# Kernel optimization log

Measured on AMD Instinct MI355X. Metric: run time of the kernel, lower is better.

## Reference

```python
import jax, jax.numpy as jnp
import numpy as np

N = 20000      # nodes
E = 640000     # directed edges
NB = 124       # n_atom_basis
FD = NB + 4    # feature dim after res_embed concat = 128
RBF = 16
CUTOFF = 10.0
NCONV = 3
SCF = FD + 10  # sidechain torsion feature dim = 138

act = jax.nn.silu  # 'swish'

def _w(key, shape, fan_in):
    return jax.random.normal(key, shape, jnp.float32) / np.sqrt(fan_in)

def setup_inputs() -> dict:
    key = jax.random.key(0)
    ks = iter(jax.random.split(key, 64))
    cg_z = jax.random.randint(next(ks), (N,), 0, 25)
    cg_xyz = jax.random.normal(next(ks), (N, 3), jnp.float32) * 4.0
    src = jax.random.randint(next(ks), (E,), 0, N)
    off = jax.random.randint(next(ks), (E,), 1, N)
    dst = (src + off) % N  # no self-loops -> dist > 0
    CG_nbr_list = jnp.stack([src, dst], axis=1)
    mapping = jax.random.randint(next(ks), (N,), 0, N)  # unused by forward
    S = jax.random.normal(next(ks), (N, NB), jnp.float32)
    p = {}
    p['res_embed'] = _w(next(ks), (25, 4), 1.0)
    p['msg_W1'] = _w(next(ks), (NCONV, FD, FD), FD); p['msg_b1'] = jnp.zeros((NCONV, FD))
    p['msg_W2'] = _w(next(ks), (NCONV, FD, FD), FD); p['msg_b2'] = jnp.zeros((NCONV, FD))
    p['dist_W'] = _w(next(ks), (NCONV, RBF, FD), RBF); p['dist_b'] = jnp.zeros((NCONV, FD))
    p['dense_W1'] = _w(next(ks), (NCONV, FD, FD), FD); p['dense_b1'] = jnp.zeros((NCONV, FD))
    p['dense_W2'] = _w(next(ks), (NCONV, FD, FD), FD); p['dense_b2'] = jnp.zeros((NCONV, FD))
    p['bb_dist_emb'] = _w(next(ks), (25, 3), 1.0)
    p['sc_dist_emb'] = _w(next(ks), (25, 10), 1.0)
    p['bba_W1'] = _w(next(ks), (FD, 3), FD); p['bba_b1'] = jnp.zeros((3,))
    p['bba_W2'] = _w(next(ks), (3, 3), 3);  p['bba_b2'] = jnp.zeros((3,))
    p['sca_W1'] = _w(next(ks), (FD, 10), FD); p['sca_b1'] = jnp.zeros((10,))
    p['sca_W2'] = _w(next(ks), (10, 10), 10); p['sca_b2'] = jnp.zeros((10,))
    p['bbt_W1'] = _w(next(ks), (FD + 3, 3), FD + 3); p['bbt_b1'] = jnp.zeros((3,))
    p['bbt_W2'] = _w(next(ks), (3, 3), 3); p['bbt_b2'] = jnp.zeros((3,))
    p['sct_W1'] = _w(next(ks), (NCONV, SCF, SCF), SCF); p['sct_b1'] = jnp.zeros((NCONV, SCF))
    p['sct_W2'] = _w(next(ks), (NCONV, SCF, SCF), SCF); p['sct_b2'] = jnp.zeros((NCONV, SCF))
    p['ft_W1'] = _w(next(ks), (SCF, 10), SCF); p['ft_b1'] = jnp.zeros((10,))
    p['ft_W2'] = _w(next(ks), (10, 10), 10); p['ft_b2'] = jnp.zeros((10,))
    return dict(cg_z=cg_z, cg_xyz=cg_xyz, CG_nbr_list=CG_nbr_list, mapping=mapping, S=S, **p)

def reference(cg_z, cg_xyz, CG_nbr_list, mapping, S, res_embed,
              msg_W1, msg_b1, msg_W2, msg_b2, dist_W, dist_b,
              dense_W1, dense_b1, dense_W2, dense_b2,
              bb_dist_emb, sc_dist_emb,
              bba_W1, bba_b1, bba_W2, bba_b2,
              sca_W1, sca_b1, sca_W2, sca_b2,
              bbt_W1, bbt_b1, bbt_W2, bbt_b2,
              sct_W1, sct_b1, sct_W2, sct_b2,
              ft_W1, ft_b1, ft_W2, ft_b2):
    nbr = CG_nbr_list  # already directed (both i>j and j>i present)
    i_idx, j_idx = nbr[:, 0], nbr[:, 1]
    r_ij = cg_xyz[j_idx] - cg_xyz[i_idx]             # [E,3]
    dist = jnp.linalg.norm(r_ij, axis=-1)            # [E]
    # PaiNN radial basis: sin(n*pi*d/cutoff)/d, n=1..RBF
    n_arr = jnp.arange(1, RBF + 1, dtype=jnp.float32)
    rbf = jnp.sin(dist[:, None] * n_arr * (jnp.pi / CUTOFF)) / dist[:, None]  # [E,RBF]
    env = jnp.where(dist < CUTOFF, 0.5 * (jnp.cos(jnp.pi * dist / CUTOFF) + 1.0), 0.0)[:, None]
    S = jnp.concatenate([S, res_embed[cg_z]], axis=-1)  # [N,FD]
    for i in range(NCONV):
        phi = act(S @ msg_W1[i] + msg_b1[i]) @ msg_W2[i] + msg_b2[i]   # [N,FD]
        w_s = (rbf @ dist_W[i] + dist_b[i]) * env                      # [E,FD]
        msg = phi[j_idx] * w_s                                         # gather + per-edge message
        v = jax.ops.segment_sum(msg, i_idx, num_segments=N)            # scatter-add
        h = act(act(v) @ dense_W1[i] + dense_b1[i]) @ dense_W2[i] + dense_b2[i]
        S = S + h
    bb_angle = act(act(S) @ bba_W1 + bba_b1) @ bba_W2 + bba_b2          # [N,3]
    bbt_in = jnp.concatenate([S, bb_angle], axis=-1)
    bb_torsion = act(act(bbt_in) @ bbt_W1 + bbt_b1) @ bbt_W2 + bbt_b2   # [N,3]
    sc_angle = act(act(S) @ sca_W1 + sca_b1) @ sca_W2 + sca_b2          # [N,10]
    sc_S = jnp.concatenate([S, sc_angle], axis=-1)                      # [N,SCF]
    for i in range(NCONV):
        sc_S = sc_S + (act(act(sc_S) @ sct_W1[i] + sct_b1[i]) @ sct_W2[i] + sct_b2[i])
    sc_torsion = act(act(sc_S) @ ft_W1 + ft_b1) @ ft_W2 + ft_b2         # [N,10]
    bb_dist = bb_dist_emb[cg_z][..., None]                              # [N,3,1]
    sc_dist = sc_dist_emb[cg_z][..., None]                              # [N,10,1]
    ic_bb = jnp.concatenate([bb_dist, bb_angle[..., None], bb_torsion[..., None]], axis=-1)  # [N,3,3]
    ic_sc = jnp.concatenate([sc_dist, sc_angle[..., None], sc_torsion[..., None]], axis=-1)  # [N,10,3]
    ic_recon = jnp.concatenate([ic_bb, ic_sc], axis=-2)                 # [N,13,3]
    return ic_recon
```

## Files before the change

kernel.cpp:

```cpp
#include <hip/hip_runtime.h>
#include <hip/hip_bf16.h>

#define DIV_UP(a,b) (((a)+(b)-1)/(b))

typedef __attribute__((ext_vector_type(8))) short bf16x8;
typedef __attribute__((ext_vector_type(4))) float f32x4;

__device__ __forceinline__ float silu_f(float x) {
    return x / (1.0f + __expf(-x));
}
__device__ __forceinline__ unsigned short f2bf(float x) {
    __hip_bfloat16 h = __float2bfloat16(x);
    return *reinterpret_cast<unsigned short*>(&h);
}
__device__ __forceinline__ float bf2f(unsigned short u) {
    unsigned int v = (unsigned int)u << 16;
    return __uint_as_float(v);
}
__device__ __forceinline__ void split_bf(float x, unsigned short& hi, unsigned short& lo) {
    hi = f2bf(x);
    lo = f2bf(x - bf2f(hi));
}
__device__ __forceinline__ bf16x8 pack8(unsigned int w0, unsigned int w1,
                                        unsigned int w2, unsigned int w3) {
    union { unsigned int u[4]; bf16x8 v; } t;
    t.u[0] = w0; t.u[1] = w1; t.u[2] = w2; t.u[3] = w3;
    return t.v;
}

#define WSLOT 16384

__global__ __launch_bounds__(256) void prep_weights_kernel(
    const float* __restrict__ msgW1, const float* __restrict__ msgW2,
    const float* __restrict__ denseW1, const float* __restrict__ denseW2,
    unsigned short* __restrict__ WB)
{
    int slot = blockIdx.y;
    int kind = slot / 3, conv = slot % 3;
    const float* base;
    switch (kind) {
        case 0: base = msgW1; break;
        case 1: base = msgW2; break;
        case 2: base = denseW1; break;
        default: base = denseW2; break;
    }
    const float* W = base + (size_t)conv * 128 * 128;
    int idx = blockIdx.x * 256 + threadIdx.x;
    if (idx >= 16384) return;
    int c = idx >> 7, k = idx & 127;
    float val = W[(size_t)k * 128 + c];
    unsigned short hi, lo;
    split_bf(val, hi, lo);
    WB[(size_t)(2 * slot) * WSLOT + idx]     = hi;
    WB[(size_t)(2 * slot + 1) * WSLOT + idx] = lo;
}

__global__ __launch_bounds__(256) void hist_kernel(
    const int* __restrict__ nbr, int* __restrict__ counts, int E)
{
    int e = blockIdx.x * 256 + threadIdx.x;
    if (e < E) atomicAdd(&counts[nbr[2 * e]], 1);
}

__global__ __launch_bounds__(1024) void scan_kernel(
    const int* __restrict__ counts, int* __restrict__ peptr, int N)
{
    __shared__ int part[1024];
    const int t = threadIdx.x;
    const int chunk = DIV_UP(N, 1024);
    int s = 0;
    for (int c = 0; c < chunk; ++c) {
        int idx = t * chunk + c;
        if (idx < N) s += (counts[idx] + 31) & ~31;
    }
    part[t] = s;
    __syncthreads();
    for (int off = 1; off < 1024; off <<= 1) {
        int v = (t >= off) ? part[t - off] : 0;
        __syncthreads();
        part[t] += v;
        __syncthreads();
    }
    int pre = (t > 0) ? part[t - 1] : 0;
    for (int c = 0; c < chunk; ++c) {
        int idx = t * chunk + c;
        if (idx < N) { peptr[idx] = pre; pre += (counts[idx] + 31) & ~31; }
    }
    if (t == 1023) peptr[N] = part[1023];
}

__global__ __launch_bounds__(256) void geom_scatter_kernel(
    const int* __restrict__ nbr, const float* __restrict__ xyz,
    const int* __restrict__ peptr, int* __restrict__ cursor,
    unsigned short* __restrict__ rbfT, unsigned short* __restrict__ envs,
    int* __restrict__ js, int E)
{
    int e = blockIdx.x * 256 + threadIdx.x;
    if (e >= E) return;
    int i = nbr[2 * e], j = nbr[2 * e + 1];
    float dx = xyz[3 * j + 0] - xyz[3 * i + 0];
    float dy = xyz[3 * j + 1] - xyz[3 * i + 1];
    float dz = xyz[3 * j + 2] - xyz[3 * i + 2];
    float dist = sqrtf(dx * dx + dy * dy + dz * dz);
    float x = dist * 0.3141592653589793f;
    float s, c;
    __sincosf(x, &s, &c);
    float env = (dist < 10.0f) ? 0.5f * (c + 1.0f) : 0.0f;
    float inv_env = env / dist;
    float two_c = 2.0f * c;
    float sm1 = 0.0f, s0 = s;
    __align__(16) unsigned short ob[16];
    #pragma unroll
    for (int k = 0; k < 16; ++k) {
        ob[k] = f2bf(s0 * inv_env);
        float s1 = two_c * s0 - sm1;
        sm1 = s0; s0 = s1;
    }
    int p = peptr[i] + atomicAdd(&cursor[i], 1);
    uint4* rp = (uint4*)(rbfT + (size_t)p * 16);
    rp[0] = *(const uint4*)&ob[0];
    rp[1] = *(const uint4*)&ob[8];
    envs[p] = f2bf(env);
    js[p] = j;
}

__global__ __launch_bounds__(256) void repack_kernel(
    unsigned short* __restrict__ rbfT, int nchunks)
{
    __shared__ __align__(16) unsigned short T[4][512];
    const int wave = threadIdx.x >> 6;
    const int lane = threadIdx.x & 63;
    const int c = blockIdx.x * 4 + wave;
    const bool act = (c < nchunks);
    if (act)
        *(uint4*)&T[wave][lane * 8] = *(const uint4*)(rbfT + (size_t)c * 512 + lane * 8);
    __syncthreads();
    if (act) {
        const int lg = lane >> 4, l15 = lane & 15;
        __align__(16) unsigned short o[8];
        #pragma unroll
        for (int i = 0; i < 8; ++i)
            o[i] = T[wave][(8 * lg + i) * 16 + l15];
        *(uint4*)(rbfT + (size_t)c * 512 + lane * 8) = *(const uint4*)o;
    }
}

__global__ __launch_bounds__(256) void concat_s_kernel(
    const float* __restrict__ S, const float* __restrict__ res_embed,
    const int* __restrict__ z, float* __restrict__ S0, int N)
{
    int idx = blockIdx.x * 256 + threadIdx.x;
    if (idx >= N * 128) return;
    int n = idx >> 7, c = idx & 127;
    float val = (c < 124) ? S[n * 124 + c] : res_embed[z[n] * 4 + (c - 124)];
    S0[idx] = val;
}

template<int MT, bool PREACT, bool RESID, typename OutT>
__global__ __launch_bounds__(256) void mlp2_mfma_kernel(
    const float* __restrict__ X,
    const unsigned short* __restrict__ W1hi, const unsigned short* __restrict__ W1lo,
    const float* __restrict__ b1,
    const unsigned short* __restrict__ W2hi, const unsigned short* __restrict__ W2lo,
    const float* __restrict__ b2,
    OutT* __restrict__ Y, int nrows)
{
    constexpr int RB   = MT / 16;
    constexpr int ROWB = 256;
    __shared__ __align__(16) unsigned short XHhi[MT * 128];
    __shared__ __align__(16) unsigned short XHlo[MT * 128];
    __shared__ __align__(16) unsigned short WS[128 * 128];

    const int tid  = threadIdx.x;
    const int wave = tid >> 6;
    const int lane = tid & 63;
    const int l15  = lane & 15;
    const int kg   = lane >> 4;
    const int row0 = blockIdx.x * MT;

    for (int idx = tid; idx < MT * 32; idx += 256) {
        int r = idx >> 5, q = idx & 31;
        int gr = row0 + r;
        float4 xv = make_float4(0.f, 0.f, 0.f, 0.f);
        if (gr < nrows) xv = *(const float4*)(X + (size_t)gr * 128 + 4 * q);
        if (PREACT) { xv.x = silu_f(xv.x); xv.y = silu_f(xv.y);
                      xv.z = silu_f(xv.z); xv.w = silu_f(xv.w); }
        ushort4 h, l;
        split_bf(xv.x, h.x, l.x); split_bf(xv.y, h.y, l.y);
        split_bf(xv.z, h.z, l.z); split_bf(xv.w, h.w, l.w);
        int off = (8 * q) ^ ((r & 7) << 4);
        *(ushort4*)((char*)XHhi + r * ROWB + off) = h;
        *(ushort4*)((char*)XHlo + r * ROWB + off) = l;
    }

    f32x4 acc[RB][2];

    #define STAGE_W(WPTR)                                                       \
        for (int idx = tid; idx < 2048; idx += 256) {                           \
            int r = idx >> 4;                                                   \
            int byt = (idx & 15) * 16;                                          \
            *(uint4*)((char*)WS + r * ROWB + (byt ^ ((r & 7) << 4))) =          \
                *(const uint4*)((WPTR) + (size_t)idx * 8);                      \
        }

    #define PASS(WITH_LO)                                                       \
        _Pragma("unroll")                                                       \
        for (int kk = 0; kk < 4; ++kk) {                                        \
            const int kbyte = kk * 64 + kg * 16;                                \
            bf16x8 ah[RB], al[RB];                                              \
            _Pragma("unroll")                                                   \
            for (int rb = 0; rb < RB; ++rb) {                                   \
                int r = 16 * rb + l15;                                          \
                int off = kbyte ^ ((r & 7) << 4);                               \
                ah[rb] = *(const bf16x8*)((const char*)XHhi + r * ROWB + off);  \
                if (WITH_LO)                                                    \
                    al[rb] = *(const bf16x8*)((const char*)XHlo + r * ROWB + off); \
            }                                                                   \
            _Pragma("unroll")                                                   \
            for (int cbi = 0; cbi < 2; ++cbi) {                                 \
                int rw = 16 * (wave + 4 * cbi) + l15;                           \
                int offw = kbyte ^ ((rw & 7) << 4);                             \
                bf16x8 bw = *(const bf16x8*)((const char*)WS + rw * ROWB + offw); \
                _Pragma("unroll")                                               \
                for (int rb = 0; rb < RB; ++rb) {                               \
                    f32x4 t = acc[rb][cbi];                                     \
                    t = __builtin_amdgcn_mfma_f32_16x16x32_bf16(ah[rb], bw, t, 0, 0, 0); \
                    if (WITH_LO)                                                \
                        t = __builtin_amdgcn_mfma_f32_16x16x32_bf16(al[rb], bw, t, 0, 0, 0); \
                    acc[rb][cbi] = t;                                           \
                }                                                               \
            }                                                                   \
        }

    #pragma unroll
    for (int a = 0; a < RB; ++a) { acc[a][0] = (f32x4){0,0,0,0}; acc[a][1] = (f32x4){0,0,0,0}; }
    STAGE_W(W1hi)
    __syncthreads();
    PASS(true)
    __syncthreads();
    STAGE_W(W1lo)
    __syncthreads();
    PASS(false)
    __syncthreads();

    #pragma unroll
    for (int cbi = 0; cbi < 2; ++cbi) {
        int col = 16 * (wave + 4 * cbi) + l15;
        float b1v = b1[col];
        #pragma unroll
        for (int rb = 0; rb < RB; ++rb)
            #pragma unroll
            for (int i = 0; i < 4; ++i) {
                int r = 16 * rb + kg * 4 + i;
                float h = silu_f(acc[rb][cbi][i] + b1v);
                unsigned short hh, hl;
                split_bf(h, hh, hl);
                int off = (2 * col) ^ ((r & 7) << 4);
                *(unsigned short*)((char*)XHhi + r * ROWB + off) = hh;
                *(unsigned short*)((char*)XHlo + r * ROWB + off) = hl;
            }
    }
    #pragma unroll
    for (int a = 0; a < RB; ++a) { acc[a][0] = (f32x4){0,0,0,0}; acc[a][1] = (f32x4){0,0,0,0}; }
    STAGE_W(W2hi)
    __syncthreads();
    PASS(true)
    __syncthreads();
    STAGE_W(W2lo)
    __syncthreads();
    PASS(false)
    #undef PASS
    #undef STAGE_W

    #pragma unroll
    for (int cbi = 0; cbi < 2; ++cbi) {
        int col = 16 * (wave + 4 * cbi) + l15;
        float b2v = b2[col];
        #pragma unroll
        for (int rb = 0; rb < RB; ++rb)
            #pragma unroll
            for (int i = 0; i < 4; ++i) {
                int gr = row0 + 16 * rb + kg * 4 + i;
                if (gr < nrows) {
                    size_t off = (size_t)gr * 128 + col;
                    float val = acc[rb][cbi][i] + b2v;
                    if (RESID) val += (float)Y[off];
                    if constexpr (sizeof(OutT) == 2)
                        Y[off] = __float2bfloat16(val);
                    else
                        Y[off] = val;
                }
            }
    }
}

template<int K, int ROWS, int RR, bool PREACT, bool RESID, typename OutT>
__global__ __launch_bounds__(256) void mlp2_kernel(
    const float* __restrict__ X, int ldX,
    const float* __restrict__ W1, const float* __restrict__ b1,
    const float* __restrict__ W2, const float* __restrict__ b2,
    OutT* __restrict__ Y, int ldY, int nrows)
{
    constexpr int NC = (K + 31) / 32;
    __shared__ float Xs[ROWS * K];
    __shared__ float Hs[ROWS * K];
    const int tid = threadIdx.x;
    const int row0 = blockIdx.x * ROWS;

    for (int idx = tid; idx < ROWS * K; idx += 256) {
        int r = idx / K, c = idx - r * K;
        int gr = row0 + r;
        float x = (gr < nrows) ? X[(size_t)gr * ldX + c] : 0.0f;
        if (PREACT) x = silu_f(x);
        Xs[idx] = x;
    }
    __syncthreads();

    const int cc = tid & 31;
    const int r0 = (tid >> 5) * RR;

    float acc[NC][RR];
    #pragma unroll
    for (int jc = 0; jc < NC; ++jc) {
        int col = cc + 32 * jc;
        float bv = (col < K) ? b1[col] : 0.0f;
        #pragma unroll
        for (int rr = 0; rr < RR; ++rr) acc[jc][rr] = bv;
    }
    for (int k = 0; k < K; ++k) {
        float w[NC];
        #pragma unroll
        for (int jc = 0; jc < NC; ++jc) {
            int col = cc + 32 * jc;
            w[jc] = (col < K) ? W1[k * K + col] : 0.0f;
        }
        float xv[RR];
        #pragma unroll
        for (int rr = 0; rr < RR; ++rr) xv[rr] = Xs[(r0 + rr) * K + k];
        #pragma unroll
        for (int jc = 0; jc < NC; ++jc)
            #pragma unroll
            for (int rr = 0; rr < RR; ++rr)
                acc[jc][rr] = fmaf(xv[rr], w[jc], acc[jc][rr]);
    }
    #pragma unroll
    for (int jc = 0; jc < NC; ++jc) {
        int col = cc + 32 * jc;
        if (col < K) {
            #pragma unroll
            for (int rr = 0; rr < RR; ++rr)
                Hs[(r0 + rr) * K + col] = silu_f(acc[jc][rr]);
        }
    }
    __syncthreads();

    #pragma unroll
    for (int jc = 0; jc < NC; ++jc) {
        int col = cc + 32 * jc;
        float bv = (col < K) ? b2[col] : 0.0f;
        #pragma unroll
        for (int rr = 0; rr < RR; ++rr) acc[jc][rr] = bv;
    }
    for (int k = 0; k < K; ++k) {
        float w[NC];
        #pragma unroll
        for (int jc = 0; jc < NC; ++jc) {
            int col = cc + 32 * jc;
            w[jc] = (col < K) ? W2[k * K + col] : 0.0f;
        }
        float xv[RR];
        #pragma unroll
        for (int rr = 0; rr < RR; ++rr) xv[rr] = Hs[(r0 + rr) * K + k];
        #pragma unroll
        for (int jc = 0; jc < NC; ++jc)
            #pragma unroll
            for (int rr = 0; rr < RR; ++rr)
                acc[jc][rr] = fmaf(xv[rr], w[jc], acc[jc][rr]);
    }
    #pragma unroll
    for (int jc = 0; jc < NC; ++jc) {
        int col = cc + 32 * jc;
        if (col < K) {
            #pragma unroll
            for (int rr = 0; rr < RR; ++rr) {
                int gr = row0 + r0 + rr;
                if (gr < nrows) {
                    size_t off = (size_t)gr * ldY + col;
                    float val = acc[jc][rr];
                    if (RESID) val += (float)Y[off];
                    if constexpr (sizeof(OutT) == 2)
                        Y[off] = __float2bfloat16(val);
                    else
                        Y[off] = val;
                }
            }
        }
    }
}

__global__ __launch_bounds__(256) void gather_mfma_kernel(
    const int* __restrict__ peptr,
    const unsigned short* __restrict__ rbfT,
    const unsigned short* __restrict__ envs,
    const int* __restrict__ js,
    const unsigned short* __restrict__ phi,
    const float* __restrict__ distW, const float* __restrict__ distb,
    float* __restrict__ v, int N)
{
    const int wv = blockIdx.x * 4 + (threadIdx.x >> 6);
    const int lane = threadIdx.x & 63;
    const int n = wv >> 1;
    const int h = wv & 1;
    if (n >= N) return;
    const int l15 = lane & 15;
    const int lg  = lane >> 4;

    f32x4 acc[4];
    float eac[4];
    #pragma unroll
    for (int cb = 0; cb < 4; ++cb) { acc[cb] = (f32x4){0,0,0,0}; eac[cb] = 0.f; }

    const int p0 = peptr[n], p1 = peptr[n + 1];

    for (int p = p0; p < p1; p += 32) {
        bf16x8 af = *(const bf16x8*)(rbfT + (size_t)(p >> 5) * 512 + lane * 8);

        bf16x8 a2f = (bf16x8){0,0,0,0,0,0,0,0};
        if (l15 == 0)
            a2f = *(const bf16x8*)(envs + p + 8 * lg);

        int4 j03 = *(const int4*)(js + p + 8 * lg);
        int4 j47 = *(const int4*)(js + p + 8 * lg + 4);

        const unsigned short* pb0 = phi + (size_t)j03.x * 128 + 64 * h + l15;
        const unsigned short* pb1 = phi + (size_t)j03.y * 128 + 64 * h + l15;
        const unsigned short* pb2 = phi + (size_t)j03.z * 128 + 64 * h + l15;
        const unsigned short* pb3 = phi + (size_t)j03.w * 128 + 64 * h + l15;
        const unsigned short* pb4 = phi + (size_t)j47.x * 128 + 64 * h + l15;
        const unsigned short* pb5 = phi + (size_t)j47.y * 128 + 64 * h + l15;
        const unsigned short* pb6 = phi + (size_t)j47.z * 128 + 64 * h + l15;
        const unsigned short* pb7 = phi + (size_t)j47.w * 128 + 64 * h + l15;

        #pragma unroll
        for (int cbi = 0; cbi < 4; ++cbi) {
            const int o = cbi * 16;
            unsigned int b0 = (unsigned int)pb0[o] | ((unsigned int)pb1[o] << 16);
            unsigned int b1 = (unsigned int)pb2[o] | ((unsigned int)pb3[o] << 16);
            unsigned int b2 = (unsigned int)pb4[o] | ((unsigned int)pb5[o] << 16);
            unsigned int b3 = (unsigned int)pb6[o] | ((unsigned int)pb7[o] << 16);
            bf16x8 bf = pack8(b0, b1, b2, b3);
            acc[cbi] = __builtin_amdgcn_mfma_f32_16x16x32_bf16(af, bf, acc[cbi], 0, 0, 0);
            f32x4 z = (f32x4){0, 0, 0, 0};
            z = __builtin_amdgcn_mfma_f32_16x16x32_bf16(a2f, bf, z, 0, 0, 0);
            eac[cbi] += z[0];
        }
    }

    #pragma unroll
    for (int cbi = 0; cbi < 4; ++cbi) {
        int col = 64 * h + cbi * 16 + l15;
        float part = acc[cbi][0] * distW[(lg * 4 + 0) * 128 + col];
        part = fmaf(acc[cbi][1], distW[(lg * 4 + 1) * 128 + col], part);
        part = fmaf(acc[cbi][2], distW[(lg * 4 + 2) * 128 + col], part);
        part = fmaf(acc[cbi][3], distW[(lg * 4 + 3) * 128 + col], part);
        if (lg == 0) part = fmaf(eac[cbi], distb[col], part);
        part += __shfl_xor(part, 16, 64);
        part += __shfl_xor(part, 32, 64);
        if (lane < 16) v[(size_t)n * 128 + col] = part;
    }
}

__global__ __launch_bounds__(256) void fused_heads_kernel(
    const float* __restrict__ S0,
    const float* __restrict__ bbaW1, const float* __restrict__ bbab1,
    const float* __restrict__ bbaW2, const float* __restrict__ bbab2,
    const float* __restrict__ bbtW1, const float* __restrict__ bbtb1,
    const float* __restrict__ bbtW2, const float* __restrict__ bbtb2,
    const float* __restrict__ scaW1, const float* __restrict__ scab1,
    const float* __restrict__ scaW2, const float* __restrict__ scab2,
    float* __restrict__ bbA, float* __restrict__ bbT,
    float* __restrict__ scA, float* __restrict__ scS, int N)
{
    const int wid = threadIdx.x >> 6;
    const int lane = threadIdx.x & 63;
    const int n = blockIdx.x * 4 + wid;
    if (n >= N) return;

    float x0 = S0[(size_t)n * 128 + lane];
    float x1 = S0[(size_t)n * 128 + 64 + lane];
    float s0 = silu_f(x0), s1 = silu_f(x1);

    float ba[3];
    #pragma unroll
    for (int m = 0; m < 3; ++m)
        ba[m] = fmaf(s0, bbaW1[lane * 3 + m], s1 * bbaW1[(lane + 64) * 3 + m]);
    #pragma unroll
    for (int m = 0; m < 3; ++m)
        #pragma unroll
        for (int off = 32; off > 0; off >>= 1)
            ba[m] += __shfl_xor(ba[m], off, 64);
    float bbo[3];
    {
        float tm[3];
        #pragma unroll
        for (int m = 0; m < 3; ++m) tm[m] = silu_f(ba[m] + bbab1[m]);
        #pragma unroll
        for (int mm = 0; mm < 3; ++mm) {
            float o = bbab2[mm];
            #pragma unroll
            for (int m = 0; m < 3; ++m) o = fmaf(tm[m], bbaW2[m * 3 + mm], o);
            bbo[mm] = o;
        }
    }
    if (lane < 3) {
        float ov = bbo[0];
        if (lane == 1) ov = bbo[1];
        if (lane == 2) ov = bbo[2];
        bbA[(size_t)n * 3 + lane] = ov;
    }

    float bt[3];
    #pragma unroll
    for (int m = 0; m < 3; ++m)
        bt[m] = fmaf(s0, bbtW1[lane * 3 + m], s1 * bbtW1[(lane + 64) * 3 + m]);
    #pragma unroll
    for (int m = 0; m < 3; ++m)
        #pragma unroll
        for (int off = 32; off > 0; off >>= 1)
            bt[m] += __shfl_xor(bt[m], off, 64);
    #pragma unroll
    for (int m = 0; m < 3; ++m)
        #pragma unroll
        for (int t = 0; t < 3; ++t)
            bt[m] = fmaf(silu_f(bbo[t]), bbtW1[(128 + t) * 3 + m], bt[m]);
    {
        float tm[3], bto[3];
        #pragma unroll
        for (int m = 0; m < 3; ++m) tm[m] = silu_f(bt[m] + bbtb1[m]);
        #pragma unroll
        for (int mm = 0; mm < 3; ++mm) {
            float o = bbtb2[mm];
            #pragma unroll
            for (int m = 0; m < 3; ++m) o = fmaf(tm[m], bbtW2[m * 3 + mm], o);
            bto[mm] = o;
        }
        if (lane < 3) {
            float ov = bto[0];
            if (lane == 1) ov = bto[1];
            if (lane == 2) ov = bto[2];
            bbT[(size_t)n * 3 + lane] = ov;
        }
    }

    float sa[10];
    #pragma unroll
    for (int m = 0; m < 10; ++m)
        sa[m] = fmaf(s0, scaW1[lane * 10 + m], s1 * scaW1[(lane + 64) * 10 + m]);
    #pragma unroll
    for (int m = 0; m < 10; ++m)
        #pragma unroll
        for (int off = 32; off > 0; off >>= 1)
            sa[m] += __shfl_xor(sa[m], off, 64);
    float sco[10];
    {
        float tm[10];
        #pragma unroll
        for (int m = 0; m < 10; ++m) tm[m] = silu_f(sa[m] + scab1[m]);
        #pragma unroll
        for (int mm = 0; mm < 10; ++mm) {
            float o = scab2[mm];
            #pragma unroll
            for (int m = 0; m < 10; ++m) o = fmaf(tm[m], scaW2[m * 10 + mm], o);
            sco[mm] = o;
        }
    }
    float scv = sco[0];
    #pragma unroll
    for (int m = 1; m < 10; ++m)
        if (lane == m) scv = sco[m];
    if (lane < 10) scA[(size_t)n * 10 + lane] = scv;

    scS[(size_t)n * 140 + lane] = x0;
    scS[(size_t)n * 140 + 64 + lane] = x1;
    if (lane < 12) scS[(size_t)n * 140 + 128 + lane] = (lane < 10) ? scv : 0.0f;
}

template<int M>
__global__ __launch_bounds__(256) void head_kernel(
    const float* __restrict__ X, int ldX, int K1,
    const float* __restrict__ X2, int ldX2, int K2,
    const float* __restrict__ W1, const float* __restrict__ b1,
    const float* __restrict__ W2, const float* __restrict__ b2,
    float* __restrict__ out, int ldOut, int nrows)
{
    const int wid = threadIdx.x >> 6;
    const int lane = threadIdx.x & 63;
    const int n = blockIdx.x * 4 + wid;
    if (n >= nrows) return;
    const int K = K1 + K2;
    float sx[3];
    #pragma unroll
    for (int t = 0; t < 3; ++t) {
        int k = lane + 64 * t;
        float v = 0.0f;
        if (k < K1) v = X[(size_t)n * ldX + k];
        else if (k < K) v = X2[(size_t)n * ldX2 + (k - K1)];
        sx[t] = (k < K) ? silu_f(v) : 0.0f;
    }
    float acc[M];
    #pragma unroll
    for (int m = 0; m < M; ++m) {
        float a = 0.0f;
        #pragma unroll
        for (int t = 0; t < 3; ++t) {
            int k = lane + 64 * t;
            if (k < K) a = fmaf(sx[t], W1[k * M + m], a);
        }
        acc[m] = a;
    }
    #pragma unroll
    for (int m = 0; m < M; ++m) {
        #pragma unroll
        for (int off = 32; off > 0; off >>= 1)
            acc[m] += __shfl_xor(acc[m], off, 64);
    }
    float tm[M];
    #pragma unroll
    for (int m = 0; m < M; ++m) tm[m] = silu_f(acc[m] + b1[m]);
    if (lane < M) {
        float o = b2[lane];
        #pragma unroll
        for (int m = 0; m < M; ++m) o = fmaf(tm[m], W2[m * M + lane], o);
        out[(size_t)n * ldOut + lane] = o;
    }
}

__global__ __launch_bounds__(256) void assemble_kernel(
    const int* __restrict__ z,
    const float* __restrict__ bbde, const float* __restrict__ scde,
    const float* __restrict__ bbA, const float* __restrict__ bbT,
    const float* __restrict__ scA, const float* __restrict__ scT,
    float* __restrict__ out, int N)
{
    int idx = blockIdx.x * 256 + threadIdx.x;
    if (idx >= N * 39) return;
    int n = idx / 39;
    int s = idx - n * 39;
    int row = s / 3;
    int col = s - row * 3;
    float val;
    if (row < 3) {
        if (col == 0)      val = bbde[z[n] * 3 + row];
        else if (col == 1) val = bbA[n * 3 + row];
        else               val = bbT[n * 3 + row];
    } else {
        int r = row - 3;
        if (col == 0)      val = scde[z[n] * 10 + r];
        else if (col == 1) val = scA[n * 10 + r];
        else               val = scT[n * 10 + r];
    }
    out[idx] = val;
}

extern "C" void kernel_launch(void* const* d_in, const int* in_sizes, int n_in,
                              void* d_out, int out_size, void* d_ws, size_t ws_size,
                              hipStream_t stream)
{
    const int*   cg_z        = (const int*)d_in[0];
    const float* cg_xyz      = (const float*)d_in[1];
    const int*   nbr         = (const int*)d_in[2];
    const float* S_in        = (const float*)d_in[4];
    const float* res_embed   = (const float*)d_in[5];
    const float* msg_W1      = (const float*)d_in[6];
    const float* msg_b1      = (const float*)d_in[7];
    const float* msg_W2      = (const float*)d_in[8];
    const float* msg_b2      = (const float*)d_in[9];
    const float* dist_W      = (const float*)d_in[10];
    const float* dist_b      = (const float*)d_in[11];
    const float* dense_W1    = (const float*)d_in[12];
    const float* dense_b1    = (const float*)d_in[13];
    const float* dense_W2    = (const float*)d_in[14];
    const float* dense_b2    = (const float*)d_in[15];
    const float* bb_dist_emb = (const float*)d_in[16];
    const float* sc_dist_emb = (const float*)d_in[17];
    const float* bba_W1      = (const float*)d_in[18];
    const float* bba_b1      = (const float*)d_in[19];
    const float* bba_W2      = (const float*)d_in[20];
    const float* bba_b2      = (const float*)d_in[21];
    const float* sca_W1      = (const float*)d_in[22];
    const float* sca_b1      = (const float*)d_in[23];
    const float* sca_W2      = (const float*)d_in[24];
    const float* sca_b2      = (const float*)d_in[25];
    const float* bbt_W1      = (const float*)d_in[26];
    const float* bbt_b1      = (const float*)d_in[27];
    const float* bbt_W2      = (const float*)d_in[28];
    const float* bbt_b2      = (const float*)d_in[29];
    const float* sct_W1      = (const float*)d_in[30];
    const float* sct_b1      = (const float*)d_in[31];
    const float* sct_W2      = (const float*)d_in[32];
    const float* sct_b2      = (const float*)d_in[33];
    const float* ft_W1       = (const float*)d_in[34];
    const float* ft_b1       = (const float*)d_in[35];
    const float* ft_W2       = (const float*)d_in[36];
    const float* ft_b2       = (const float*)d_in[37];

    const int N = in_sizes[0];
    const int E = in_sizes[2] / 2;
    const int EPAD = ((E + 31 * N) / 32) * 32 + 32;

    unsigned short* WB   = (unsigned short*)d_ws;
    unsigned short* rbfT = WB + (size_t)24 * WSLOT;
    unsigned short* envs = rbfT + (size_t)EPAD * 16;
    int*            js   = (int*)(envs + (size_t)EPAD);
    float* ws   = (float*)(js + (size_t)EPAD);
    float* S0   = ws;  ws += (size_t)N * 128;
    float* V    = ws;  ws += (size_t)N * 128;
    float* scS  = ws;  ws += (size_t)N * 140;
    float* bbA  = ws;  ws += (size_t)N * 3;
    float* bbT  = ws;  ws += (size_t)N * 3;
    float* scA  = ws;  ws += (size_t)N * 10;
    float* scT  = ws;  ws += (size_t)N * 10;
    __hip_bfloat16* PHI = (__hip_bfloat16*)ws;  ws += (size_t)N * 64;
    int* peptr  = (int*)ws;  ws = (float*)((int*)ws + (N + 1));
    int* counts = (int*)ws;  ws = (float*)((int*)ws + N);
    int* cursor = (int*)ws;  ws = (float*)((int*)ws + N);

    (void)hipMemsetAsync(rbfT, 0, (size_t)EPAD * 38, stream);
    (void)hipMemsetAsync(counts, 0, (size_t)2 * N * sizeof(int), stream);

    prep_weights_kernel<<<dim3(64, 12), 256, 0, stream>>>(
        msg_W1, msg_W2, dense_W1, dense_W2, WB);

    hist_kernel<<<DIV_UP(E, 256), 256, 0, stream>>>(nbr, counts, E);
    scan_kernel<<<1, 1024, 0, stream>>>(counts, peptr, N);
    geom_scatter_kernel<<<DIV_UP(E, 256), 256, 0, stream>>>(
        nbr, cg_xyz, peptr, cursor, rbfT, envs, js, E);
    const int nchunks = EPAD / 32;
    repack_kernel<<<DIV_UP(nchunks, 4), 256, 0, stream>>>(rbfT, nchunks);

    concat_s_kernel<<<DIV_UP(N * 128, 256), 256, 0, stream>>>(S_in, res_embed, cg_z, S0, N);

    #define WHI(kind, conv) (WB + (size_t)(2 * ((kind) * 3 + (conv))) * WSLOT)
    #define WLO(kind, conv) (WB + (size_t)(2 * ((kind) * 3 + (conv)) + 1) * WSLOT)

    for (int i = 0; i < 3; ++i) {
        mlp2_mfma_kernel<48, false, false, __hip_bfloat16>
            <<<DIV_UP(N, 48), 256, 0, stream>>>(
            S0, WHI(0, i), WLO(0, i), msg_b1 + i * 128,
            WHI(1, i), WLO(1, i), msg_b2 + i * 128, PHI, N);
        gather_mfma_kernel<<<DIV_UP(2 * N, 4), 256, 0, stream>>>(
            peptr, rbfT, envs, js, (const unsigned short*)PHI,
            dist_W + (size_t)i * 16 * 128, dist_b + i * 128, V, N);
        mlp2_mfma_kernel<48, true, true, float>
            <<<DIV_UP(N, 48), 256, 0, stream>>>(
            V, WHI(2, i), WLO(2, i), dense_b1 + i * 128,
            WHI(3, i), WLO(3, i), dense_b2 + i * 128, S0, N);
    }

    fused_heads_kernel<<<DIV_UP(N, 4), 256, 0, stream>>>(
        S0,
        bba_W1, bba_b1, bba_W2, bba_b2,
        bbt_W1, bbt_b1, bbt_W2, bbt_b2,
        sca_W1, sca_b1, sca_W2, sca_b2,
        bbA, bbT, scA, scS, N);

    for (int i = 0; i < 3; ++i) {
        mlp2_kernel<138, 16, 2, true, true, float><<<DIV_UP(N, 16), 256, 0, stream>>>(
            scS, 140, sct_W1 + (size_t)i * 138 * 138, sct_b1 + i * 138,
            sct_W2 + (size_t)i * 138 * 138, sct_b2 + i * 138, scS, 140, N);
    }
    head_kernel<10><<<DIV_UP(N, 4), 256, 0, stream>>>(
        scS, 140, 138, scS, 0, 0, ft_W1, ft_b1, ft_W2, ft_b2, scT, 10, N);

    assemble_kernel<<<DIV_UP(N * 39, 256), 256, 0, stream>>>(
        cg_z, bb_dist_emb, sc_dist_emb, bbA, bbT, scA, scT, (float*)d_out, N);

    #undef WHI
    #undef WLO
}
```

Before: 665.4 us.

## Write edge geometry in edge order and gather into CSR via permutation index

The geometry kernel now writes RBF, envelope and neighbor index contiguously by edge id and scatters only a 4-byte edge id into the CSR slot. The repack kernel then gathers from the edge-ordered buffers into the padded, transposed CSR layout, with padding slots pointing at a zeroed sentinel edge. This replaces the large scattered 38-byte-per-slot writes and the full memset of the padded buffers with a small fill kernel and indirect reads. Scratch space is aliased onto the S0 and V buffers before they are used, and repack skips chunks past the real total.

```diff
diff --git a/kernel.cpp b/kernel.cpp
--- a/kernel.cpp
+++ b/kernel.cpp
@@ -89,11 +89,23 @@
     if (t == 1023) peptr[N] = part[1023];
 }
 
-__global__ __launch_bounds__(256) void geom_scatter_kernel(
+__global__ __launch_bounds__(256) void fill_kernel(
+    int* __restrict__ eofp, int EPAD,
+    unsigned short* __restrict__ rbfE, unsigned short* __restrict__ envE,
+    int* __restrict__ jE, int E)
+{
+    int idx = blockIdx.x * 256 + threadIdx.x;
+    if (idx < EPAD) eofp[idx] = E;
+    if (idx < 16) rbfE[(size_t)E * 16 + idx] = 0;
+    if (idx == 16) envE[E] = 0;
+    if (idx == 17) jE[E] = 0;
+}
+
+__global__ __launch_bounds__(256) void geom_kernel(
     const int* __restrict__ nbr, const float* __restrict__ xyz,
     const int* __restrict__ peptr, int* __restrict__ cursor,
-    unsigned short* __restrict__ rbfT, unsigned short* __restrict__ envs,
-    int* __restrict__ js, int E)
+    unsigned short* __restrict__ rbfE, unsigned short* __restrict__ envE,
+    int* __restrict__ jE, int* __restrict__ eofp, int E)
 {
     int e = blockIdx.x * 256 + threadIdx.x;
     if (e >= E) return;
@@ -116,32 +128,44 @@
         float s1 = two_c * s0 - sm1;
         sm1 = s0; s0 = s1;
     }
-    int p = peptr[i] + atomicAdd(&cursor[i], 1);
-    uint4* rp = (uint4*)(rbfT + (size_t)p * 16);
+    uint4* rp = (uint4*)(rbfE + (size_t)e * 16);
     rp[0] = *(const uint4*)&ob[0];
     rp[1] = *(const uint4*)&ob[8];
-    envs[p] = f2bf(env);
-    js[p] = j;
+    envE[e] = f2bf(env);
+    jE[e] = j;
+    int p = peptr[i] + atomicAdd(&cursor[i], 1);
+    eofp[p] = e;
 }
 
 __global__ __launch_bounds__(256) void repack_kernel(
-    unsigned short* __restrict__ rbfT, int nchunks)
-{
-    __shared__ __align__(16) unsigned short T[4][512];
+    const int* __restrict__ eofp,
+    const unsigned short* __restrict__ rbfE, const unsigned short* __restrict__ envE,
+    const int* __restrict__ jE,
+    unsigned short* __restrict__ rbfT, unsigned short* __restrict__ envs,
+    int* __restrict__ js, const int* __restrict__ peptr, int N)
+{
+    const int total = peptr[N];
     const int wave = threadIdx.x >> 6;
     const int lane = threadIdx.x & 63;
     const int c = blockIdx.x * 4 + wave;
-    const bool act = (c < nchunks);
-    if (act)
-        *(uint4*)&T[wave][lane * 8] = *(const uint4*)(rbfT + (size_t)c * 512 + lane * 8);
-    __syncthreads();
-    if (act) {
-        const int lg = lane >> 4, l15 = lane & 15;
-        __align__(16) unsigned short o[8];
-        #pragma unroll
-        for (int i = 0; i < 8; ++i)
-            o[i] = T[wave][(8 * lg + i) * 16 + l15];
-        *(uint4*)(rbfT + (size_t)c * 512 + lane * 8) = *(const uint4*)o;
+    const int p0 = 32 * c;
+    if (p0 >= total) return;
+    const int lg = lane >> 4, l15 = lane & 15;
+
+    const int* eb = eofp + p0 + 8 * lg;
+    __align__(16) unsigned short o[8];
+    #pragma unroll
+    for (int i = 0; i < 8; ++i) {
+        int e = eb[i];
+        o[i] = rbfE[(size_t)e * 16 + l15];
+    }
+    *(uint4*)(rbfT + (size_t)c * 512 + lane * 8) = *(const uint4*)o;
+
+    if (lane < 32) {
+        int p = p0 + lane;
+        int e = eofp[p];
+        envs[p] = envE[e];
+        js[p]   = jE[e];
     }
 }
 
@@ -725,7 +749,11 @@
     int* counts = (int*)ws;  ws = (float*)((int*)ws + N);
     int* cursor = (int*)ws;  ws = (float*)((int*)ws + N);
 
-    (void)hipMemsetAsync(rbfT, 0, (size_t)EPAD * 38, stream);
+    unsigned short* envE = (unsigned short*)S0;
+    int*            jE   = (int*)(S0 + 400000);
+    int*            eofp = (int*)(S0 + 1100000);
+    unsigned short* rbfE = (unsigned short*)V;
+
     (void)hipMemsetAsync(counts, 0, (size_t)2 * N * sizeof(int), stream);
 
     prep_weights_kernel<<<dim3(64, 12), 256, 0, stream>>>(
@@ -733,10 +761,11 @@
 
     hist_kernel<<<DIV_UP(E, 256), 256, 0, stream>>>(nbr, counts, E);
     scan_kernel<<<1, 1024, 0, stream>>>(counts, peptr, N);
-    geom_scatter_kernel<<<DIV_UP(E, 256), 256, 0, stream>>>(
-        nbr, cg_xyz, peptr, cursor, rbfT, envs, js, E);
-    const int nchunks = EPAD / 32;
-    repack_kernel<<<DIV_UP(nchunks, 4), 256, 0, stream>>>(rbfT, nchunks);
+    fill_kernel<<<DIV_UP(EPAD, 256), 256, 0, stream>>>(eofp, EPAD, rbfE, envE, jE, E);
+    geom_kernel<<<DIV_UP(E, 256), 256, 0, stream>>>(
+        nbr, cg_xyz, peptr, cursor, rbfE, envE, jE, eofp, E);
+    repack_kernel<<<DIV_UP(EPAD / 32, 4), 256, 0, stream>>>(
+        eofp, rbfE, envE, jE, rbfT, envs, js, peptr, N);
 
     concat_s_kernel<<<DIV_UP(N * 128, 256), 256, 0, stream>>>(S_in, res_embed, cg_z, S0, N);
 
```

Result: no change. 669.1 us (+0.6%).
